# Kernel tuning notes

Hardware: AMD Instinct MI355X
Metric: run time of the kernel (lower is better)

## Reference

```python
import jax, jax.numpy as jnp
import numpy as np

N_NODES = 200000
N_EDGES = 800000
D = 128


def setup_inputs() -> dict:
    key = jax.random.key(0)
    ks = jax.random.split(key, 6)
    x = jax.random.normal(ks[0], (N_NODES, D), dtype=jnp.float32)
    edge_attr = jax.random.normal(ks[1], (N_EDGES, D), dtype=jnp.float32)
    edge_index = jax.random.randint(ks[2], (2, N_EDGES), 0, N_NODES, dtype=jnp.int64)
    # model_fn: MLP(concat_dim=2D -> D -> D) with ReLU
    W1 = jax.random.normal(ks[3], (2 * D, D), dtype=jnp.float32) * (1.0 / np.sqrt(2 * D))
    b1 = jnp.zeros((D,), dtype=jnp.float32)
    W2 = jax.random.normal(ks[4], (D, D), dtype=jnp.float32) * (1.0 / np.sqrt(D))
    b2 = jnp.zeros((D,), dtype=jnp.float32)
    return {"x": x, "edge_attr": edge_attr, "edge_index": edge_index,
            "W1": W1, "b1": b1, "W2": W2, "b2": b2}


def reference(x, edge_attr, edge_index, W1, b1, W2, b2):
    # scatter_add edge features onto receiver nodes (edge_index[1])
    receivers = edge_index[1]
    agg = jax.ops.segment_sum(edge_attr, receivers, num_segments=x.shape[0])  # [N, D]
    node_inputs = jnp.concatenate([x, agg], axis=-1)  # [N, 2D]
    h = jax.nn.relu(node_inputs @ W1 + b1)
    x_new = h @ W2 + b2  # [N, D]
    return x_new
```

## Files before the change

### kernel.cpp

```cpp
#include <hip/hip_runtime.h>

#define D 128
#define NPB 32

typedef __attribute__((ext_vector_type(8))) short short8;
typedef __attribute__((ext_vector_type(4))) float f32x4;

__device__ inline unsigned short f2bf(float f) {
    unsigned int u = __float_as_uint(f);
    u += 0x7fffu + ((u >> 16) & 1u);
    return (unsigned short)(u >> 16);
}

__global__ __launch_bounds__(256) void pack_weights_kernel(
    const float* __restrict__ W1, const float* __restrict__ W2,
    unsigned short* __restrict__ pW1, unsigned short* __restrict__ pW2)
{
    int idx = blockIdx.x * 256 + threadIdx.x;
    if (idx < 32768) {
        int j = idx & 7, lane = (idx >> 3) & 63, s = (idx >> 9) & 7, c = idx >> 12;
        int k = s * 32 + ((lane >> 4) << 3) + j;
        int n = (c << 4) + (lane & 15);
        pW1[idx] = f2bf(W1[k * D + n]);
    } else if (idx < 49152) {
        int i2 = idx - 32768;
        int j = i2 & 7, lane = (i2 >> 3) & 63, s = (i2 >> 9) & 3, c = i2 >> 11;
        int k = s * 32 + ((lane >> 4) << 3) + j;
        int n = (c << 4) + (lane & 15);
        pW2[i2] = f2bf(W2[k * D + n]);
    }
}

__global__ __launch_bounds__(256) void hist_kernel(
    const int* __restrict__ recv, int* __restrict__ counts, int n_edges)
{
    int e = blockIdx.x * 256 + threadIdx.x;
    if (e < n_edges) atomicAdd(&counts[recv[e]], 1);
}

__global__ __launch_bounds__(256) void reduce_kernel(
    const int* __restrict__ counts, int* __restrict__ blocksum, int n)
{
    __shared__ int s[256];
    int t = threadIdx.x, i = blockIdx.x * 256 + t;
    s[t] = (i < n) ? counts[i] : 0;
    __syncthreads();
    for (int off = 128; off > 0; off >>= 1) {
        if (t < off) s[t] += s[t + off];
        __syncthreads();
    }
    if (t == 0) blocksum[blockIdx.x] = s[0];
}

__global__ __launch_bounds__(1024) void scanblk_kernel(
    const int* __restrict__ blocksum, int* __restrict__ blockoff, int nblocks)
{
    __shared__ int s[1024];
    int t = threadIdx.x;
    int v = (t < nblocks) ? blocksum[t] : 0;
    s[t] = v;
    __syncthreads();
    for (int off = 1; off < 1024; off <<= 1) {
        int add = (t >= off) ? s[t - off] : 0;
        __syncthreads();
        s[t] += add;
        __syncthreads();
    }
    if (t < nblocks) blockoff[t] = s[t] - v;
}

__global__ __launch_bounds__(256) void scan_kernel(
    const int* __restrict__ counts, const int* __restrict__ blockoff,
    int* __restrict__ starts, int* __restrict__ cursor, int n)
{
    __shared__ int s[256];
    int t = threadIdx.x, i = blockIdx.x * 256 + t;
    int v = (i < n) ? counts[i] : 0;
    s[t] = v;
    __syncthreads();
    for (int off = 1; off < 256; off <<= 1) {
        int add = (t >= off) ? s[t - off] : 0;
        __syncthreads();
        s[t] += add;
        __syncthreads();
    }
    int excl = s[t] - v + blockoff[blockIdx.x];
    if (i < n) {
        starts[i] = excl;
        cursor[i] = excl;
        if (i == n - 1) starts[n] = excl + v;
    }
}

__global__ __launch_bounds__(256) void reorder_kernel(
    const int* __restrict__ recv, int* __restrict__ cursor,
    int* __restrict__ edge_ids, int n_edges)
{
    int e = blockIdx.x * 256 + threadIdx.x;
    if (e < n_edges) {
        int r = recv[e];
        int pos = atomicAdd(&cursor[r], 1);
        edge_ids[pos] = e;
    }
}

__global__ __launch_bounds__(256) void mlp_kernel(
    const float* __restrict__ x, const float* __restrict__ edge_attr,
    const int* __restrict__ starts, const int* __restrict__ edge_ids,
    const unsigned short* __restrict__ pW1, const unsigned short* __restrict__ pW2,
    const float* __restrict__ b1, const float* __restrict__ b2,
    float* __restrict__ out, int n_nodes)
{
    __shared__ unsigned short in_s[NPB][2 * D + 8];
    __shared__ unsigned short h_s[NPB][D + 8];

    const int t = threadIdx.x;
    const int node0 = blockIdx.x * NPB;

    for (int i = t; i < NPB * 32; i += 256) {
        int m = i >> 5, c4 = i & 31;
        int node = node0 + m;
        float4 v = make_float4(0.f, 0.f, 0.f, 0.f);
        if (node < n_nodes) v = *(const float4*)(x + (size_t)node * D + c4 * 4);
        ushort4 b;
        b.x = f2bf(v.x); b.y = f2bf(v.y); b.z = f2bf(v.z); b.w = f2bf(v.w);
        *(ushort4*)(&in_s[m][c4 * 4]) = b;
    }

    {
        int g = t >> 5, l32 = t & 31;
        for (int i = 0; i < 4; ++i) {
            int m = g * 4 + i;
            int node = node0 + m;
            float4 acc = make_float4(0.f, 0.f, 0.f, 0.f);
            if (node < n_nodes) {
                int p = starts[node], pe = starts[node + 1];
                for (; p + 1 < pe; p += 2) {
                    int e0 = edge_ids[p], e1 = edge_ids[p + 1];
                    float4 v0 = *(const float4*)(edge_attr + (size_t)e0 * D + l32 * 4);
                    float4 v1 = *(const float4*)(edge_attr + (size_t)e1 * D + l32 * 4);
                    acc.x += v0.x + v1.x; acc.y += v0.y + v1.y;
                    acc.z += v0.z + v1.z; acc.w += v0.w + v1.w;
                }
                if (p < pe) {
                    int e0 = edge_ids[p];
                    float4 v0 = *(const float4*)(edge_attr + (size_t)e0 * D + l32 * 4);
                    acc.x += v0.x; acc.y += v0.y; acc.z += v0.z; acc.w += v0.w;
                }
            }
            ushort4 b;
            b.x = f2bf(acc.x); b.y = f2bf(acc.y); b.z = f2bf(acc.z); b.w = f2bf(acc.w);
            *(ushort4*)(&in_s[m][D + l32 * 4]) = b;
        }
    }
    __syncthreads();

    const int w = t >> 6, l = t & 63;
    const int col = l & 15, quad = l >> 4;
    const int c0 = w * 2, c1 = c0 + 1;

    f32x4 a00, a01, a10, a11;
    {
        float bA = b1[c0 * 16 + col], bB = b1[c1 * 16 + col];
        a00 = (f32x4){bA, bA, bA, bA}; a01 = (f32x4){bB, bB, bB, bB};
        a10 = a00; a11 = a01;
    }
#pragma unroll
    for (int s = 0; s < 8; ++s) {
        short8 fa0 = *(const short8*)(&in_s[col][s * 32 + quad * 8]);
        short8 fa1 = *(const short8*)(&in_s[16 + col][s * 32 + quad * 8]);
        short8 fb0 = *(const short8*)(pW1 + (((c0 * 8 + s) * 64 + l) * 8));
        short8 fb1 = *(const short8*)(pW1 + (((c1 * 8 + s) * 64 + l) * 8));
        a00 = __builtin_amdgcn_mfma_f32_16x16x32_bf16(fa0, fb0, a00, 0, 0, 0);
        a01 = __builtin_amdgcn_mfma_f32_16x16x32_bf16(fa0, fb1, a01, 0, 0, 0);
        a10 = __builtin_amdgcn_mfma_f32_16x16x32_bf16(fa1, fb0, a10, 0, 0, 0);
        a11 = __builtin_amdgcn_mfma_f32_16x16x32_bf16(fa1, fb1, a11, 0, 0, 0);
    }
#pragma unroll
    for (int r = 0; r < 4; ++r) {
        int row = quad * 4 + r;
        h_s[row][c0 * 16 + col]      = f2bf(fmaxf(a00[r], 0.f));
        h_s[row][c1 * 16 + col]      = f2bf(fmaxf(a01[r], 0.f));
        h_s[16 + row][c0 * 16 + col] = f2bf(fmaxf(a10[r], 0.f));
        h_s[16 + row][c1 * 16 + col] = f2bf(fmaxf(a11[r], 0.f));
    }
    __syncthreads();

    f32x4 o00, o01, o10, o11;
    {
        float bA = b2[c0 * 16 + col], bB = b2[c1 * 16 + col];
        o00 = (f32x4){bA, bA, bA, bA}; o01 = (f32x4){bB, bB, bB, bB};
        o10 = o00; o11 = o01;
    }
#pragma unroll
    for (int s = 0; s < 4; ++s) {
        short8 fa0 = *(const short8*)(&h_s[col][s * 32 + quad * 8]);
        short8 fa1 = *(const short8*)(&h_s[16 + col][s * 32 + quad * 8]);
        short8 fb0 = *(const short8*)(pW2 + (((c0 * 4 + s) * 64 + l) * 8));
        short8 fb1 = *(const short8*)(pW2 + (((c1 * 4 + s) * 64 + l) * 8));
        o00 = __builtin_amdgcn_mfma_f32_16x16x32_bf16(fa0, fb0, o00, 0, 0, 0);
        o01 = __builtin_amdgcn_mfma_f32_16x16x32_bf16(fa0, fb1, o01, 0, 0, 0);
        o10 = __builtin_amdgcn_mfma_f32_16x16x32_bf16(fa1, fb0, o10, 0, 0, 0);
        o11 = __builtin_amdgcn_mfma_f32_16x16x32_bf16(fa1, fb1, o11, 0, 0, 0);
    }
#pragma unroll
    for (int r = 0; r < 4; ++r) {
        int row = quad * 4 + r;
        int na = node0 + row, nb = node0 + 16 + row;
        if (na < n_nodes) {
            out[(size_t)na * D + c0 * 16 + col] = o00[r];
            out[(size_t)na * D + c1 * 16 + col] = o01[r];
        }
        if (nb < n_nodes) {
            out[(size_t)nb * D + c0 * 16 + col] = o10[r];
            out[(size_t)nb * D + c1 * 16 + col] = o11[r];
        }
    }
}

extern "C" void kernel_launch(void* const* d_in, const int* in_sizes, int n_in,
                              void* d_out, int out_size, void* d_ws, size_t ws_size,
                              hipStream_t stream) {
    const float* x         = (const float*)d_in[0];
    const float* edge_attr = (const float*)d_in[1];
    const int*   edge_index= (const int*)d_in[2];
    const float* W1        = (const float*)d_in[3];
    const float* b1        = (const float*)d_in[4];
    const float* W2        = (const float*)d_in[5];
    const float* b2        = (const float*)d_in[6];
    float* out = (float*)d_out;

    const int n_nodes = in_sizes[0] / D;
    const int n_edges = in_sizes[1] / D;
    const int* recv = edge_index + n_edges;

    char* wsb = (char*)d_ws;
    int* counts   = (int*)(wsb + 0);
    int* cursor   = (int*)(wsb + (1u << 20));
    int* starts   = (int*)(wsb + (2u << 20));
    int* blocksum = (int*)(wsb + (3u << 20));
    int* blockoff = (int*)(wsb + (3u << 20) + (1u << 16));
    int* edge_ids = (int*)(wsb + (4u << 20));
    unsigned short* pW1 = (unsigned short*)(wsb + (8u << 20));
    unsigned short* pW2 = (unsigned short*)(wsb + (8u << 20) + (1u << 17));

    hipMemsetAsync(counts, 0, (size_t)n_nodes * sizeof(int), stream);

    pack_weights_kernel<<<192, 256, 0, stream>>>(W1, W2, pW1, pW2);

    const int eb = (n_edges + 255) / 256;
    hist_kernel<<<eb, 256, 0, stream>>>(recv, counts, n_edges);

    const int nb = (n_nodes + 255) / 256;
    reduce_kernel<<<nb, 256, 0, stream>>>(counts, blocksum, n_nodes);
    scanblk_kernel<<<1, 1024, 0, stream>>>(blocksum, blockoff, nb);
    scan_kernel<<<nb, 256, 0, stream>>>(counts, blockoff, starts, cursor, n_nodes);
    reorder_kernel<<<eb, 256, 0, stream>>>(recv, cursor, edge_ids, n_edges);

    mlp_kernel<<<(n_nodes + NPB - 1) / NPB, 256, 0, stream>>>(
        x, edge_attr, starts, edge_ids, pW1, pW2, b1, b2, out, n_nodes);
}
```

Baseline: 760.8 us.

## Balance edge gather across block via LDS float atomics; fuse memset and scan launches

The per-node gather, where each 32-lane group walked four nodes' edge lists, becomes a flat loop over the block's contiguous edge range. Each edge is accumulated into an fp32 shared-memory buffer with LDS atomics, which needs a new sorted receivers array written by the reorder kernel. The aim is to remove load imbalance from degree variation. The memset is folded into the weight-pack kernel, and the single-block scan launch is replaced by each scan block redundantly summing prior block sums. Together these cut launches at the cost of extra LDS atomic traffic and redundant global reads.

```diff
diff --git a/kernel.cpp b/kernel.cpp
--- a/kernel.cpp
+++ b/kernel.cpp
@@ -12,9 +12,10 @@
     return (unsigned short)(u >> 16);
 }
 
-__global__ __launch_bounds__(256) void pack_weights_kernel(
+__global__ __launch_bounds__(256) void setup_kernel(
     const float* __restrict__ W1, const float* __restrict__ W2,
-    unsigned short* __restrict__ pW1, unsigned short* __restrict__ pW2)
+    unsigned short* __restrict__ pW1, unsigned short* __restrict__ pW2,
+    int* __restrict__ counts, int n_nodes)
 {
     int idx = blockIdx.x * 256 + threadIdx.x;
     if (idx < 32768) {
@@ -29,6 +30,7 @@
         int n = (c << 4) + (lane & 15);
         pW2[i2] = f2bf(W2[k * D + n]);
     }
+    for (int i = idx; i < n_nodes; i += gridDim.x * 256) counts[i] = 0;
 }
 
 __global__ __launch_bounds__(256) void hist_kernel(
@@ -52,29 +54,24 @@
     if (t == 0) blocksum[blockIdx.x] = s[0];
 }
 
-__global__ __launch_bounds__(1024) void scanblk_kernel(
-    const int* __restrict__ blocksum, int* __restrict__ blockoff, int nblocks)
-{
-    __shared__ int s[1024];
-    int t = threadIdx.x;
-    int v = (t < nblocks) ? blocksum[t] : 0;
-    s[t] = v;
-    __syncthreads();
-    for (int off = 1; off < 1024; off <<= 1) {
-        int add = (t >= off) ? s[t - off] : 0;
-        __syncthreads();
-        s[t] += add;
-        __syncthreads();
-    }
-    if (t < nblocks) blockoff[t] = s[t] - v;
-}
-
 __global__ __launch_bounds__(256) void scan_kernel(
-    const int* __restrict__ counts, const int* __restrict__ blockoff,
+    const int* __restrict__ counts, const int* __restrict__ blocksum,
     int* __restrict__ starts, int* __restrict__ cursor, int n)
 {
     __shared__ int s[256];
-    int t = threadIdx.x, i = blockIdx.x * 256 + t;
+    int t = threadIdx.x, b = blockIdx.x, i = b * 256 + t;
+
+    int acc = 0;
+    for (int j = t; j < b; j += 256) acc += blocksum[j];
+    s[t] = acc;
+    __syncthreads();
+    for (int off = 128; off > 0; off >>= 1) {
+        if (t < off) s[t] += s[t + off];
+        __syncthreads();
+    }
+    int blockoff = s[0];
+    __syncthreads();
+
     int v = (i < n) ? counts[i] : 0;
     s[t] = v;
     __syncthreads();
@@ -84,7 +81,7 @@
         s[t] += add;
         __syncthreads();
     }
-    int excl = s[t] - v + blockoff[blockIdx.x];
+    int excl = s[t] - v + blockoff;
     if (i < n) {
         starts[i] = excl;
         cursor[i] = excl;
@@ -94,28 +91,33 @@
 
 __global__ __launch_bounds__(256) void reorder_kernel(
     const int* __restrict__ recv, int* __restrict__ cursor,
-    int* __restrict__ edge_ids, int n_edges)
+    int* __restrict__ edge_ids, int* __restrict__ recvs, int n_edges)
 {
     int e = blockIdx.x * 256 + threadIdx.x;
     if (e < n_edges) {
         int r = recv[e];
         int pos = atomicAdd(&cursor[r], 1);
         edge_ids[pos] = e;
+        recvs[pos] = r;
     }
 }
 
 __global__ __launch_bounds__(256) void mlp_kernel(
     const float* __restrict__ x, const float* __restrict__ edge_attr,
     const int* __restrict__ starts, const int* __restrict__ edge_ids,
+    const int* __restrict__ recvs,
     const unsigned short* __restrict__ pW1, const unsigned short* __restrict__ pW2,
     const float* __restrict__ b1, const float* __restrict__ b2,
     float* __restrict__ out, int n_nodes)
 {
     __shared__ unsigned short in_s[NPB][2 * D + 8];
-    __shared__ unsigned short h_s[NPB][D + 8];
+    __shared__ float agg[NPB][D];
+    unsigned short (*h_s)[D + 8] = (unsigned short (*)[D + 8])(&agg[0][0]);
 
     const int t = threadIdx.x;
     const int node0 = blockIdx.x * NPB;
+
+    for (int i = t; i < NPB * D; i += 256) (&agg[0][0])[i] = 0.f;
 
     for (int i = t; i < NPB * 32; i += 256) {
         int m = i >> 5, c4 = i & 31;
@@ -126,32 +128,34 @@
         b.x = f2bf(v.x); b.y = f2bf(v.y); b.z = f2bf(v.z); b.w = f2bf(v.w);
         *(ushort4*)(&in_s[m][c4 * 4]) = b;
     }
+    __syncthreads();
 
     {
-        int g = t >> 5, l32 = t & 31;
-        for (int i = 0; i < 4; ++i) {
-            int m = g * 4 + i;
-            int node = node0 + m;
-            float4 acc = make_float4(0.f, 0.f, 0.f, 0.f);
-            if (node < n_nodes) {
-                int p = starts[node], pe = starts[node + 1];
-                for (; p + 1 < pe; p += 2) {
-                    int e0 = edge_ids[p], e1 = edge_ids[p + 1];
-                    float4 v0 = *(const float4*)(edge_attr + (size_t)e0 * D + l32 * 4);
-                    float4 v1 = *(const float4*)(edge_attr + (size_t)e1 * D + l32 * 4);
-                    acc.x += v0.x + v1.x; acc.y += v0.y + v1.y;
-                    acc.z += v0.z + v1.z; acc.w += v0.w + v1.w;
-                }
-                if (p < pe) {
-                    int e0 = edge_ids[p];
-                    float4 v0 = *(const float4*)(edge_attr + (size_t)e0 * D + l32 * 4);
-                    acc.x += v0.x; acc.y += v0.y; acc.z += v0.z; acc.w += v0.w;
-                }
-            }
-            ushort4 b;
-            b.x = f2bf(acc.x); b.y = f2bf(acc.y); b.z = f2bf(acc.z); b.w = f2bf(acc.w);
-            *(ushort4*)(&in_s[m][D + l32 * 4]) = b;
+        int nhi = node0 + NPB; if (nhi > n_nodes) nhi = n_nodes;
+        const int e0 = starts[node0];
+        const int e1 = starts[nhi];
+        const int g = t >> 5, l32 = t & 31;
+#pragma unroll 2
+        for (int p = e0 + g; p < e1; p += 8) {
+            int e = edge_ids[p];
+            int r = recvs[p] - node0;
+            float4 v = *(const float4*)(edge_attr + (size_t)e * D + l32 * 4);
+            atomicAdd(&agg[r][l32],      v.x);
+            atomicAdd(&agg[r][32 + l32], v.y);
+            atomicAdd(&agg[r][64 + l32], v.z);
+            atomicAdd(&agg[r][96 + l32], v.w);
         }
+    }
+    __syncthreads();
+
+    for (int i = t; i < NPB * 32; i += 256) {
+        int m = i >> 5, q = i & 31;
+        ushort4 b;
+        b.x = f2bf(agg[m][q]);
+        b.y = f2bf(agg[m][32 + q]);
+        b.z = f2bf(agg[m][64 + q]);
+        b.w = f2bf(agg[m][96 + q]);
+        *(ushort4*)(&in_s[m][D + q * 4]) = b;
     }
     __syncthreads();
 
@@ -239,24 +243,21 @@
     int* cursor   = (int*)(wsb + (1u << 20));
     int* starts   = (int*)(wsb + (2u << 20));
     int* blocksum = (int*)(wsb + (3u << 20));
-    int* blockoff = (int*)(wsb + (3u << 20) + (1u << 16));
     int* edge_ids = (int*)(wsb + (4u << 20));
-    unsigned short* pW1 = (unsigned short*)(wsb + (8u << 20));
-    unsigned short* pW2 = (unsigned short*)(wsb + (8u << 20) + (1u << 17));
-
-    hipMemsetAsync(counts, 0, (size_t)n_nodes * sizeof(int), stream);
-
-    pack_weights_kernel<<<192, 256, 0, stream>>>(W1, W2, pW1, pW2);
+    int* recvs_s  = (int*)(wsb + (8u << 20));
+    unsigned short* pW1 = (unsigned short*)(wsb + (12u << 20));
+    unsigned short* pW2 = (unsigned short*)(wsb + (12u << 20) + (1u << 17));
+
+    setup_kernel<<<400, 256, 0, stream>>>(W1, W2, pW1, pW2, counts, n_nodes);
 
     const int eb = (n_edges + 255) / 256;
     hist_kernel<<<eb, 256, 0, stream>>>(recv, counts, n_edges);
 
     const int nb = (n_nodes + 255) / 256;
     reduce_kernel<<<nb, 256, 0, stream>>>(counts, blocksum, n_nodes);
-    scanblk_kernel<<<1, 1024, 0, stream>>>(blocksum, blockoff, nb);
-    scan_kernel<<<nb, 256, 0, stream>>>(counts, blockoff, starts, cursor, n_nodes);
-    reorder_kernel<<<eb, 256, 0, stream>>>(recv, cursor, edge_ids, n_edges);
+    scan_kernel<<<nb, 256, 0, stream>>>(counts, blocksum, starts, cursor, n_nodes);
+    reorder_kernel<<<eb, 256, 0, stream>>>(recv, cursor, edge_ids, recvs_s, n_edges);
 
     mlp_kernel<<<(n_nodes + NPB - 1) / NPB, 256, 0, stream>>>(
-        x, edge_attr, starts, edge_ids, pW1, pW2, b1, b2, out, n_nodes);
-}
+        x, edge_attr, starts, edge_ids, recvs_s, pW1, pW2, b1, b2, out, n_nodes);
+}
```

After: 1.110 ms. 1.46x slower.

## Split edge gather into its own kernel and fold memset and block scan

Applied to the files above, without the earlier changes.

Moves the per-node edge_attr gather-sum out of the MLP kernel into a separate grid-stride gather kernel. It unrolls the loop by four edges and writes bf16 aggregates to a workspace buffer, which the MLP kernel then loads. The memset is folded into the weight-packing kernel, and the single-block scan kernel is removed: each scan block now sums the preceding block sums itself. This is meant to decouple the latency-bound gather from the MFMA kernel and cut launch count, at the cost of an extra bf16 round trip through memory (about 51MB write plus read).

```diff
diff --git a/kernel.cpp b/kernel.cpp
--- a/kernel.cpp
+++ b/kernel.cpp
@@ -12,9 +12,10 @@
     return (unsigned short)(u >> 16);
 }
 
-__global__ __launch_bounds__(256) void pack_weights_kernel(
+__global__ __launch_bounds__(256) void setup_kernel(
     const float* __restrict__ W1, const float* __restrict__ W2,
-    unsigned short* __restrict__ pW1, unsigned short* __restrict__ pW2)
+    unsigned short* __restrict__ pW1, unsigned short* __restrict__ pW2,
+    int* __restrict__ counts, int n_nodes)
 {
     int idx = blockIdx.x * 256 + threadIdx.x;
     if (idx < 32768) {
@@ -29,6 +30,7 @@
         int n = (c << 4) + (lane & 15);
         pW2[i2] = f2bf(W2[k * D + n]);
     }
+    for (int i = idx; i < n_nodes; i += gridDim.x * 256) counts[i] = 0;
 }
 
 __global__ __launch_bounds__(256) void hist_kernel(
@@ -52,29 +54,24 @@
     if (t == 0) blocksum[blockIdx.x] = s[0];
 }
 
-__global__ __launch_bounds__(1024) void scanblk_kernel(
-    const int* __restrict__ blocksum, int* __restrict__ blockoff, int nblocks)
-{
-    __shared__ int s[1024];
-    int t = threadIdx.x;
-    int v = (t < nblocks) ? blocksum[t] : 0;
-    s[t] = v;
-    __syncthreads();
-    for (int off = 1; off < 1024; off <<= 1) {
-        int add = (t >= off) ? s[t - off] : 0;
-        __syncthreads();
-        s[t] += add;
-        __syncthreads();
-    }
-    if (t < nblocks) blockoff[t] = s[t] - v;
-}
-
 __global__ __launch_bounds__(256) void scan_kernel(
-    const int* __restrict__ counts, const int* __restrict__ blockoff,
+    const int* __restrict__ counts, const int* __restrict__ blocksum,
     int* __restrict__ starts, int* __restrict__ cursor, int n)
 {
     __shared__ int s[256];
-    int t = threadIdx.x, i = blockIdx.x * 256 + t;
+    int t = threadIdx.x, b = blockIdx.x, i = b * 256 + t;
+
+    int acc = 0;
+    for (int j = t; j < b; j += 256) acc += blocksum[j];
+    s[t] = acc;
+    __syncthreads();
+    for (int off = 128; off > 0; off >>= 1) {
+        if (t < off) s[t] += s[t + off];
+        __syncthreads();
+    }
+    int blockoff = s[0];
+    __syncthreads();
+
     int v = (i < n) ? counts[i] : 0;
     s[t] = v;
     __syncthreads();
@@ -84,7 +81,7 @@
         s[t] += add;
         __syncthreads();
     }
-    int excl = s[t] - v + blockoff[blockIdx.x];
+    int excl = s[t] - v + blockoff;
     if (i < n) {
         starts[i] = excl;
         cursor[i] = excl;
@@ -104,9 +101,41 @@
     }
 }
 
+__global__ __launch_bounds__(256) void gather_kernel(
+    const float* __restrict__ edge_attr,
+    const int* __restrict__ starts, const int* __restrict__ edge_ids,
+    unsigned short* __restrict__ aggb, int n_nodes)
+{
+    const int g = threadIdx.x >> 5, l32 = threadIdx.x & 31;
+    const int stride = gridDim.x * 8;
+    for (int node = blockIdx.x * 8 + g; node < n_nodes; node += stride) {
+        int p = starts[node], pe = starts[node + 1];
+        float4 acc = make_float4(0.f, 0.f, 0.f, 0.f);
+        for (; p + 3 < pe; p += 4) {
+            int e0 = edge_ids[p], e1 = edge_ids[p + 1];
+            int e2 = edge_ids[p + 2], e3 = edge_ids[p + 3];
+            float4 v0 = *(const float4*)(edge_attr + (size_t)e0 * D + l32 * 4);
+            float4 v1 = *(const float4*)(edge_attr + (size_t)e1 * D + l32 * 4);
+            float4 v2 = *(const float4*)(edge_attr + (size_t)e2 * D + l32 * 4);
+            float4 v3 = *(const float4*)(edge_attr + (size_t)e3 * D + l32 * 4);
+            acc.x += (v0.x + v1.x) + (v2.x + v3.x);
+            acc.y += (v0.y + v1.y) + (v2.y + v3.y);
+            acc.z += (v0.z + v1.z) + (v2.z + v3.z);
+            acc.w += (v0.w + v1.w) + (v2.w + v3.w);
+        }
+        for (; p < pe; ++p) {
+            int e0 = edge_ids[p];
+            float4 v0 = *(const float4*)(edge_attr + (size_t)e0 * D + l32 * 4);
+            acc.x += v0.x; acc.y += v0.y; acc.z += v0.z; acc.w += v0.w;
+        }
+        ushort4 b;
+        b.x = f2bf(acc.x); b.y = f2bf(acc.y); b.z = f2bf(acc.z); b.w = f2bf(acc.w);
+        *(ushort4*)(aggb + (size_t)node * D + l32 * 4) = b;
+    }
+}
+
 __global__ __launch_bounds__(256) void mlp_kernel(
-    const float* __restrict__ x, const float* __restrict__ edge_attr,
-    const int* __restrict__ starts, const int* __restrict__ edge_ids,
+    const float* __restrict__ x, const unsigned short* __restrict__ aggb,
     const unsigned short* __restrict__ pW1, const unsigned short* __restrict__ pW2,
     const float* __restrict__ b1, const float* __restrict__ b2,
     float* __restrict__ out, int n_nodes)
@@ -126,32 +155,12 @@
         b.x = f2bf(v.x); b.y = f2bf(v.y); b.z = f2bf(v.z); b.w = f2bf(v.w);
         *(ushort4*)(&in_s[m][c4 * 4]) = b;
     }
-
-    {
-        int g = t >> 5, l32 = t & 31;
-        for (int i = 0; i < 4; ++i) {
-            int m = g * 4 + i;
-            int node = node0 + m;
-            float4 acc = make_float4(0.f, 0.f, 0.f, 0.f);
-            if (node < n_nodes) {
-                int p = starts[node], pe = starts[node + 1];
-                for (; p + 1 < pe; p += 2) {
-                    int e0 = edge_ids[p], e1 = edge_ids[p + 1];
-                    float4 v0 = *(const float4*)(edge_attr + (size_t)e0 * D + l32 * 4);
-                    float4 v1 = *(const float4*)(edge_attr + (size_t)e1 * D + l32 * 4);
-                    acc.x += v0.x + v1.x; acc.y += v0.y + v1.y;
-                    acc.z += v0.z + v1.z; acc.w += v0.w + v1.w;
-                }
-                if (p < pe) {
-                    int e0 = edge_ids[p];
-                    float4 v0 = *(const float4*)(edge_attr + (size_t)e0 * D + l32 * 4);
-                    acc.x += v0.x; acc.y += v0.y; acc.z += v0.z; acc.w += v0.w;
-                }
-            }
-            ushort4 b;
-            b.x = f2bf(acc.x); b.y = f2bf(acc.y); b.z = f2bf(acc.z); b.w = f2bf(acc.w);
-            *(ushort4*)(&in_s[m][D + l32 * 4]) = b;
-        }
+    for (int i = t; i < NPB * 32; i += 256) {
+        int m = i >> 5, c4 = i & 31;
+        int node = node0 + m;
+        ushort4 b = make_ushort4(0, 0, 0, 0);
+        if (node < n_nodes) b = *(const ushort4*)(aggb + (size_t)node * D + c4 * 4);
+        *(ushort4*)(&in_s[m][D + c4 * 4]) = b;
     }
     __syncthreads();
 
@@ -239,24 +248,23 @@
     int* cursor   = (int*)(wsb + (1u << 20));
     int* starts   = (int*)(wsb + (2u << 20));
     int* blocksum = (int*)(wsb + (3u << 20));
-    int* blockoff = (int*)(wsb + (3u << 20) + (1u << 16));
     int* edge_ids = (int*)(wsb + (4u << 20));
     unsigned short* pW1 = (unsigned short*)(wsb + (8u << 20));
     unsigned short* pW2 = (unsigned short*)(wsb + (8u << 20) + (1u << 17));
-
-    hipMemsetAsync(counts, 0, (size_t)n_nodes * sizeof(int), stream);
-
-    pack_weights_kernel<<<192, 256, 0, stream>>>(W1, W2, pW1, pW2);
+    unsigned short* aggb = (unsigned short*)(wsb + (16u << 20));
+
+    setup_kernel<<<400, 256, 0, stream>>>(W1, W2, pW1, pW2, counts, n_nodes);
 
     const int eb = (n_edges + 255) / 256;
     hist_kernel<<<eb, 256, 0, stream>>>(recv, counts, n_edges);
 
     const int nb = (n_nodes + 255) / 256;
     reduce_kernel<<<nb, 256, 0, stream>>>(counts, blocksum, n_nodes);
-    scanblk_kernel<<<1, 1024, 0, stream>>>(blocksum, blockoff, nb);
-    scan_kernel<<<nb, 256, 0, stream>>>(counts, blockoff, starts, cursor, n_nodes);
+    scan_kernel<<<nb, 256, 0, stream>>>(counts, blocksum, starts, cursor, n_nodes);
     reorder_kernel<<<eb, 256, 0, stream>>>(recv, cursor, edge_ids, n_edges);
 
+    gather_kernel<<<2048, 256, 0, stream>>>(edge_attr, starts, edge_ids, aggb, n_nodes);
+
     mlp_kernel<<<(n_nodes + NPB - 1) / NPB, 256, 0, stream>>>(
-        x, edge_attr, starts, edge_ids, pW1, pW2, b1, b2, out, n_nodes);
-}
+        x, aggb, pW1, pW2, b1, b2, out, n_nodes);
+}
```

Result: no change. 772.2 us (+1.5%).
